# Kernel tuning notes

Hardware: AMD Instinct MI355X
Metric: run time of the kernel (lower is better)

The kernel has to match this reference:

```python
import jax, jax.numpy as jnp
import numpy as np

B, N, K, H, C = 16, 2048, 9, 128, 2  # K = nb_neighbors, kernel_size = K+1


def setup_inputs() -> dict:
    key = jax.random.key(0)
    ks = jax.random.split(key, 7)
    s = 0.1
    x = jax.random.normal(ks[0], (B, N, C), jnp.float32)
    Wconv = jax.random.normal(ks[1], (H, C, K + 1), jnp.float32) * s  # conv1d weight
    bconv = jax.random.normal(ks[2], (H,), jnp.float32) * s
    W1 = jax.random.normal(ks[3], (H, C), jnp.float32) * s
    b1 = jax.random.normal(ks[4], (H,), jnp.float32) * s
    W2 = jax.random.normal(ks[5], (H, H), jnp.float32) * s
    b2 = jax.random.normal(ks[6], (H,), jnp.float32) * s
    return {"x": x, "Wconv": Wconv, "bconv": bconv, "W1": W1, "b1": b1, "W2": W2, "b2": b2}


def reference(x, Wconv, bconv, W1, b1, W2, b2):
    # node embedding: W1(x)
    node_emb = jnp.einsum('bnc,hc->bnh', x, W1) + b1  # (B,N,H)

    # pairwise Euclidean distances (B,N,N) via the GEMM form
    sq = jnp.sum(x * x, axis=-1)  # (B,N)
    d2 = sq[:, :, None] + sq[:, None, :] - 2.0 * jnp.einsum('bnc,bmc->bnm', x, x)
    dist = jnp.sqrt(jnp.maximum(d2, 0.0))

    # torch: topk(k=N) (descending) then take last K+1 columns -> the K+1
    # smallest distances ordered descending (nearest/self last)
    knn = jnp.flip(jnp.argsort(dist, axis=-1)[..., : K + 1], axis=-1)  # (B,N,K+1)

    # batched gather of neighbor coords: (B,N,K+1,C)
    coords = jax.vmap(lambda xb, ib: xb[ib])(x, knn)

    # conv1d with kernel spanning the full window -> single output position,
    # i.e. a contraction over (channel, position)
    conv_emb = jnp.einsum('bnkc,hck->bnh', coords, Wconv) + bconv  # (B,N,H)
    conv_emb = jnp.einsum('bnh,eh->bne', conv_emb, W2) + b2

    return node_emb + conv_emb
```

## Files before the change

### kernel.cpp

```cpp
#include <hip/hip_runtime.h>
#include <cfloat>
#include <stdint.h>

#define B_   16
#define N_   2048
#define KK   10
#define H_   128
#define SUB  32
#define NCH  (N_ / SUB)

#define RANK_BLOCKS (B_ * 32)
#define WEFF_OUT    (H_ * KK * 2 + H_)
#define WEFF_BLOCKS ((WEFF_OUT * 4) / 256)

__device__ inline uint32_t f32_ordered(float f) {
    uint32_t u = __float_as_uint(f);
    return (u & 0x80000000u) ? ~u : (u | 0x80000000u);
}

__global__ __launch_bounds__(256) void setup_kernel(
    const float* __restrict__ x,
    const float* __restrict__ Wconv, const float* __restrict__ bconv,
    const float* __restrict__ b1,    const float* __restrict__ W2,
    const float* __restrict__ b2,
    float4* __restrict__ xsorted,
    float*  __restrict__ weff,
    float*  __restrict__ btot)
{
#pragma clang fp contract(off)
    __shared__ __align__(16) uint64_t sk[N_];
    __shared__ int pcnt[4 * 64];
    const int tid = threadIdx.x;

    if (blockIdx.x >= RANK_BLOCKS) {
        const int g = (blockIdx.x - RANK_BLOCKS) * 256 + tid;
        const int o = g >> 2, q = g & 3;
        float acc = 0.f;
        if (o < H_ * KK * 2) {
            const int e = o / 20, r = o % 20, k = r >> 1, c = r & 1;
            const float* w2p = W2 + e * H_ + q * 32;
            const float* wcp = Wconv + (q * 32) * (2 * KK) + c * KK + k;
#pragma unroll 8
            for (int h = 0; h < 32; ++h)
                acc += w2p[h] * wcp[h * (2 * KK)];
        } else {
            const int e = o - H_ * KK * 2;
            const float* w2p = W2 + e * H_ + q * 32;
            const float* bcp = bconv + q * 32;
#pragma unroll 8
            for (int h = 0; h < 32; ++h) acc += w2p[h] * bcp[h];
        }
        acc += __shfl_xor(acc, 1, 64);
        acc += __shfl_xor(acc, 2, 64);
        if (q == 0) {
            if (o < H_ * KK * 2) weff[o] = acc;
            else {
                const int e = o - H_ * KK * 2;
                btot[e] = acc + b1[e] + b2[e];
            }
        }
        return;
    }

    const int b  = blockIdx.x >> 5;
    const int sg = blockIdx.x & 31;
    const float2* xb = (const float2*)(x + (size_t)b * N_ * 2);

    for (int i = tid; i < N_; i += 256)
        sk[i] = ((uint64_t)f32_ordered(xb[i].x) << 32) | (uint32_t)i;
    __syncthreads();

    const int el = tid & 63;
    const int pt = tid >> 6;
    const uint64_t kown = sk[sg * 64 + el];
    const ulonglong2* sk2 = (const ulonglong2*)sk + pt * 256;
    int cnt = 0;
#pragma unroll 2
    for (int j = 0; j < 256; j += 4) {
        ulonglong2 t0 = sk2[j + 0];
        ulonglong2 t1 = sk2[j + 1];
        ulonglong2 t2 = sk2[j + 2];
        ulonglong2 t3 = sk2[j + 3];
        cnt += (int)(t0.x < kown) + (int)(t0.y < kown)
             + (int)(t1.x < kown) + (int)(t1.y < kown)
             + (int)(t2.x < kown) + (int)(t2.y < kown)
             + (int)(t3.x < kown) + (int)(t3.y < kown);
    }
    pcnt[pt * 64 + el] = cnt;
    __syncthreads();

    if (tid < 64) {
        const int r = pcnt[tid] + pcnt[64 + tid] + pcnt[128 + tid] + pcnt[192 + tid];
        const int i = sg * 64 + tid;
        float2 p = xb[i];
        float sm = p.x * p.x + p.y * p.y;
        xsorted[(size_t)b * N_ + r] =
            make_float4(p.x, p.y, sm, __uint_as_float((uint32_t)i));
    }
}

__global__ __launch_bounds__(512, 4) void knn_conv_kernel(
    const float4* __restrict__ xsorted,
    const float* __restrict__ W1,
    const float* __restrict__ weff,
    const float* __restrict__ btot,
    float* __restrict__ out)
{
#pragma clang fp contract(off)
    __shared__ float4 xs4[N_];
    __shared__ float  wcoord[64 * 21];

    const int tid  = threadIdx.x;
    const int w    = tid >> 6;
    const int r    = tid & 7;
    const int qm   = tid >> 3;
    const int b    = blockIdx.x >> 5;
    const int tile = blockIdx.x & 31;

    const float4* xb = xsorted + (size_t)b * N_;
    for (int i = tid; i < N_; i += 512) xs4[i] = xb[i];
    __syncthreads();

    const float4 qv = xs4[tile * 64 + qm];
    const float  qx = qv.x, qy = qv.y, sqn = qv.z;
    const int    gfirst = tile * 64 + w * 8;
    const float  qa  = xs4[gfirst].x;
    const float  qbx = xs4[gfirst + 7].x;

    const uint64_t KINIT = (((uint64_t)0x7F7FFFFFu) << 32) | 0x3FFFFFu;
    uint64_t hk[KK];
#pragma unroll
    for (int j = 0; j < KK; ++j) hk[j] = KINIT;
    float h9d  = FLT_MAX;
    float shb  = FLT_MAX;
    float gate = FLT_MAX;

    auto insert = [&](float dc, float cw, int m) {
        uint32_t oi = __float_as_uint(cw);
        uint64_t key = ((uint64_t)__float_as_uint(dc) << 32)
                     | (oi << 11) | (uint32_t)m;
        if (key < hk[KK - 1]) {
#pragma unroll
            for (int j = KK - 1; j >= 1; --j) {
                bool cj  = key < hk[j];
                bool cjm = key < hk[j - 1];
                hk[j] = cj ? (cjm ? hk[j - 1] : key) : hk[j];
            }
            hk[0] = (key < hk[0]) ? key : hk[0];
        }
        h9d  = __uint_as_float((uint32_t)(hk[KK - 1] >> 32));
        gate = fminf(h9d, shb);
    };

    auto scan_chunk = [&](int mc) {
        const int m0 = mc + r;
        float4 c0 = xs4[m0 + 0];
        float4 c1 = xs4[m0 + 8];
        float4 c2 = xs4[m0 + 16];
        float4 c3 = xs4[m0 + 24];
        float dc0, dc1, dc2, dc3;
        { float s = sqn + c0.z; float pr = qx * c0.x;
          float dt = __builtin_fmaf(qy, c0.y, pr);
          float d2 = __builtin_fmaf(-2.0f, dt, s); dc0 = d2 > 0.0f ? d2 : 0.0f; }
        { float s = sqn + c1.z; float pr = qx * c1.x;
          float dt = __builtin_fmaf(qy, c1.y, pr);
          float d2 = __builtin_fmaf(-2.0f, dt, s); dc1 = d2 > 0.0f ? d2 : 0.0f; }
        { float s = sqn + c2.z; float pr = qx * c2.x;
          float dt = __builtin_fmaf(qy, c2.y, pr);
          float d2 = __builtin_fmaf(-2.0f, dt, s); dc2 = d2 > 0.0f ? d2 : 0.0f; }
        { float s = sqn + c3.z; float pr = qx * c3.x;
          float dt = __builtin_fmaf(qy, c3.y, pr);
          float d2 = __builtin_fmaf(-2.0f, dt, s); dc3 = d2 > 0.0f ? d2 : 0.0f; }
        if (dc0 <= gate) insert(dc0, c0.w, m0 + 0);
        if (dc1 <= gate) insert(dc1, c1.w, m0 + 8);
        if (dc2 <= gate) insert(dc2, c2.w, m0 + 16);
        if (dc3 <= gate) insert(dc3, c3.w, m0 + 24);
    };

    auto bounds = [&]() {
        float gb = h9d;
        gb = fminf(gb, __shfl_xor(gb, 1, 64));
        gb = fminf(gb, __shfl_xor(gb, 2, 64));
        gb = fminf(gb, __shfl_xor(gb, 4, 64));
        float h1 = __uint_as_float((uint32_t)(hk[1] >> 32));
        h1 = fmaxf(h1, __shfl_xor(h1, 1, 64));
        h1 = fmaxf(h1, __shfl_xor(h1, 2, 64));
        h1 = fmaxf(h1, __shfl_xor(h1, 4, 64));
        shb  = fminf(shb, fminf(gb, h1));
        gate = fminf(h9d, shb);
        float wm = shb;
        wm = fmaxf(wm, __shfl_xor(wm, 8,  64));
        wm = fmaxf(wm, __shfl_xor(wm, 16, 64));
        wm = fmaxf(wm, __shfl_xor(wm, 32, 64));
        return wm;
    };

    const int home = tile * 2 + (w >> 2);
    int c0s = home - 1;
    if (c0s < 0) c0s = 0;
    if (c0s > NCH - 3) c0s = NCH - 3;
    scan_chunk((c0s + 0) * SUB);
    scan_chunk((c0s + 1) * SUB);
    scan_chunk((c0s + 2) * SUB);

    {
        uint64_t tc[KK];
#pragma unroll
        for (int j = 0; j < KK; ++j) tc[j] = hk[j];
        uint64_t last = 0;
#pragma unroll
        for (int sel = 0; sel < KK; ++sel) {
            uint64_t v  = tc[0];
            uint64_t t1 = __shfl_xor((unsigned long long)v, 1, 64);
            uint64_t m1 = v  < t1 ? v  : t1;
            uint64_t t2 = __shfl_xor((unsigned long long)m1, 2, 64);
            uint64_t m2 = m1 < t2 ? m1 : t2;
            uint64_t t4 = __shfl_xor((unsigned long long)m2, 4, 64);
            uint64_t vm = m2 < t4 ? m2 : t4;
            if (v == vm) {
#pragma unroll
                for (int j = 0; j < KK - 1; ++j) tc[j] = tc[j + 1];
                tc[KK - 1] = 0xFFFFFFFFFFFFFFFFull;
            }
            last = vm;
        }
        shb  = __uint_as_float((uint32_t)(last >> 32));
        gate = fminf(h9d, shb);
    }

    int  cl = c0s - 1, cr = c0s + 3;
    bool la = (cl >= 0), ra = (cr <= NCH - 1);
    while (la || ra) {
        float wm = bounds();
        if (la) {
            float gl = qa - xs4[cl * SUB + SUB - 1].x;
            if (__builtin_fmaf(gl, gl, -4e-6f) > wm) la = false;
            else { scan_chunk(cl * SUB); cl -= 1; la = (cl >= 0); }
        }
        if (ra) {
            float gr = xs4[cr * SUB].x - qbx;
            if (__builtin_fmaf(gr, gr, -4e-6f) > wm) ra = false;
            else { scan_chunk(cr * SUB); cr += 1; ra = (cr <= NCH - 1); }
        }
    }

    const int e = tid & 127;
    float we[20];
    {
        const float4* wp = (const float4*)(weff + e * 20);
#pragma unroll
        for (int rr = 0; rr < 5; ++rr) {
            float4 v = wp[rr];
            we[4 * rr + 0] = v.x; we[4 * rr + 1] = v.y;
            we[4 * rr + 2] = v.z; we[4 * rr + 3] = v.w;
        }
    }
    const float w1x = W1[e * 2 + 0];
    const float w1y = W1[e * 2 + 1];
    const float bt  = btot[e];

    {
#pragma unroll
        for (int sel = 0; sel < KK; ++sel) {
            uint64_t v  = hk[0];
            uint64_t t1 = __shfl_xor((unsigned long long)v, 1, 64);
            uint64_t m1 = v  < t1 ? v  : t1;
            uint64_t t2 = __shfl_xor((unsigned long long)m1, 2, 64);
            uint64_t m2 = m1 < t2 ? m1 : t2;
            uint64_t t4 = __shfl_xor((unsigned long long)m2, 4, 64);
            uint64_t vm = m2 < t4 ? m2 : t4;
            if (v == vm) {
#pragma unroll
                for (int j = 0; j < KK - 1; ++j) hk[j] = hk[j + 1];
                hk[KK - 1] = 0xFFFFFFFFFFFFFFFFull;
            }
            if (r == 0) {
                float4 c = xs4[(int)(vm & 0x7FF)];
                const int k = (KK - 1) - sel;
                wcoord[qm * 21 + 2 * k + 0] = c.x;
                wcoord[qm * 21 + 2 * k + 1] = c.y;
            }
        }
    }
    __syncthreads();

    const int qb_ = tid >> 7;
    const size_t obase = (size_t)b * N_ * H_;
#pragma unroll
    for (int jj = 0; jj < 16; ++jj) {
        const int qq = qb_ + 4 * jj;
        float4 xq = xs4[tile * 64 + qq];
        uint32_t orig = __float_as_uint(xq.w);
        const float* wc = &wcoord[qq * 21];
        float acc = bt;
        acc += xq.x * w1x;
        acc += xq.y * w1y;
#pragma unroll
        for (int k = 0; k < KK; ++k) {
            acc += wc[2 * k + 0] * we[2 * k + 0];
            acc += wc[2 * k + 1] * we[2 * k + 1];
        }
        out[obase + (size_t)orig * H_ + e] = acc;
    }
}

extern "C" void kernel_launch(void* const* d_in, const int* in_sizes, int n_in,
                              void* d_out, int out_size, void* d_ws, size_t ws_size,
                              hipStream_t stream) {
    const float* x     = (const float*)d_in[0];
    const float* Wconv = (const float*)d_in[1];
    const float* bconv = (const float*)d_in[2];
    const float* W1    = (const float*)d_in[3];
    const float* b1    = (const float*)d_in[4];
    const float* W2    = (const float*)d_in[5];
    const float* b2    = (const float*)d_in[6];
    float* out  = (float*)d_out;
    float* weff = (float*)d_ws;
    float* btot = weff + H_ * KK * 2;
    float4* xsorted = (float4*)((char*)d_ws + 16384);

    setup_kernel<<<dim3(RANK_BLOCKS + WEFF_BLOCKS), dim3(256), 0, stream>>>(
        x, Wconv, bconv, b1, W2, b2, xsorted, weff, btot);
    knn_conv_kernel<<<dim3(B_ * (N_ / 64)), dim3(512), 0, stream>>>(
        xsorted, W1, weff, btot, out);
}
```

Before: 143.6 us.

## Split each query's KNN scan across 16 lanes and halve queries per block

Each block now handles 32 queries instead of 64, with 16 lanes per query instead of 8, so the grid doubles and every lane scans half as many candidates per chunk. The wave reductions gain one extra shuffle stage to merge 16 partial top-K lists, and the launch bound asks for 8 waves per SIMD instead of 4. Sentinel keys now carry the lane id so they stay distinct during the merge. The goal is more parallelism and shorter per-lane serial insert chains, paid for by extra shuffle merges, more blocks each reloading the whole batch's points into shared memory, and tighter register limits.

After: 148.5 us. +3.4%, slower.

```diff
diff --git a/kernel.cpp b/kernel.cpp
--- a/kernel.cpp
+++ b/kernel.cpp
@@ -99,7 +99,7 @@
     }
 }
 
-__global__ __launch_bounds__(512, 4) void knn_conv_kernel(
+__global__ __launch_bounds__(512, 8) void knn_conv_kernel(
     const float4* __restrict__ xsorted,
     const float* __restrict__ W1,
     const float* __restrict__ weff,
@@ -108,29 +108,30 @@
 {
 #pragma clang fp contract(off)
     __shared__ float4 xs4[N_];
-    __shared__ float  wcoord[64 * 21];
+    __shared__ float  wcoord[32 * 21];
 
     const int tid  = threadIdx.x;
     const int w    = tid >> 6;
-    const int r    = tid & 7;
-    const int qm   = tid >> 3;
-    const int b    = blockIdx.x >> 5;
-    const int tile = blockIdx.x & 31;
+    const int l    = tid & 63;
+    const int r    = tid & 15;
+    const int qm   = tid >> 4;
+    const int b    = blockIdx.x >> 6;
+    const int tile = blockIdx.x & 63;
 
     const float4* xb = xsorted + (size_t)b * N_;
     for (int i = tid; i < N_; i += 512) xs4[i] = xb[i];
     __syncthreads();
 
-    const float4 qv = xs4[tile * 64 + qm];
+    const float4 qv = xs4[tile * 32 + qm];
     const float  qx = qv.x, qy = qv.y, sqn = qv.z;
-    const int    gfirst = tile * 64 + w * 8;
+    const int    gfirst = tile * 32 + w * 4;
     const float  qa  = xs4[gfirst].x;
-    const float  qbx = xs4[gfirst + 7].x;
-
-    const uint64_t KINIT = (((uint64_t)0x7F7FFFFFu) << 32) | 0x3FFFFFu;
+    const float  qbx = xs4[gfirst + 3].x;
+
+    const uint64_t KSENT = (((uint64_t)0x7F7FFFFFu) << 32) | 0x400000u | (uint32_t)l;
     uint64_t hk[KK];
 #pragma unroll
-    for (int j = 0; j < KK; ++j) hk[j] = KINIT;
+    for (int j = 0; j < KK; ++j) hk[j] = KSENT;
     float h9d  = FLT_MAX;
     float shb  = FLT_MAX;
     float gate = FLT_MAX;
@@ -155,26 +156,16 @@
     auto scan_chunk = [&](int mc) {
         const int m0 = mc + r;
         float4 c0 = xs4[m0 + 0];
-        float4 c1 = xs4[m0 + 8];
-        float4 c2 = xs4[m0 + 16];
-        float4 c3 = xs4[m0 + 24];
-        float dc0, dc1, dc2, dc3;
+        float4 c1 = xs4[m0 + 16];
+        float dc0, dc1;
         { float s = sqn + c0.z; float pr = qx * c0.x;
           float dt = __builtin_fmaf(qy, c0.y, pr);
           float d2 = __builtin_fmaf(-2.0f, dt, s); dc0 = d2 > 0.0f ? d2 : 0.0f; }
         { float s = sqn + c1.z; float pr = qx * c1.x;
           float dt = __builtin_fmaf(qy, c1.y, pr);
           float d2 = __builtin_fmaf(-2.0f, dt, s); dc1 = d2 > 0.0f ? d2 : 0.0f; }
-        { float s = sqn + c2.z; float pr = qx * c2.x;
-          float dt = __builtin_fmaf(qy, c2.y, pr);
-          float d2 = __builtin_fmaf(-2.0f, dt, s); dc2 = d2 > 0.0f ? d2 : 0.0f; }
-        { float s = sqn + c3.z; float pr = qx * c3.x;
-          float dt = __builtin_fmaf(qy, c3.y, pr);
-          float d2 = __builtin_fmaf(-2.0f, dt, s); dc3 = d2 > 0.0f ? d2 : 0.0f; }
         if (dc0 <= gate) insert(dc0, c0.w, m0 + 0);
-        if (dc1 <= gate) insert(dc1, c1.w, m0 + 8);
-        if (dc2 <= gate) insert(dc2, c2.w, m0 + 16);
-        if (dc3 <= gate) insert(dc3, c3.w, m0 + 24);
+        if (dc1 <= gate) insert(dc1, c1.w, m0 + 16);
     };
 
     auto bounds = [&]() {
@@ -182,21 +173,21 @@
         gb = fminf(gb, __shfl_xor(gb, 1, 64));
         gb = fminf(gb, __shfl_xor(gb, 2, 64));
         gb = fminf(gb, __shfl_xor(gb, 4, 64));
+        gb = fminf(gb, __shfl_xor(gb, 8, 64));
         float h1 = __uint_as_float((uint32_t)(hk[1] >> 32));
         h1 = fmaxf(h1, __shfl_xor(h1, 1, 64));
         h1 = fmaxf(h1, __shfl_xor(h1, 2, 64));
         h1 = fmaxf(h1, __shfl_xor(h1, 4, 64));
+        h1 = fmaxf(h1, __shfl_xor(h1, 8, 64));
         shb  = fminf(shb, fminf(gb, h1));
         gate = fminf(h9d, shb);
         float wm = shb;
-        wm = fmaxf(wm, __shfl_xor(wm, 8,  64));
         wm = fmaxf(wm, __shfl_xor(wm, 16, 64));
         wm = fmaxf(wm, __shfl_xor(wm, 32, 64));
         return wm;
     };
 
-    const int home = tile * 2 + (w >> 2);
-    int c0s = home - 1;
+    int c0s = tile - 1;
     if (c0s < 0) c0s = 0;
     if (c0s > NCH - 3) c0s = NCH - 3;
     scan_chunk((c0s + 0) * SUB);
@@ -216,7 +207,9 @@
             uint64_t t2 = __shfl_xor((unsigned long long)m1, 2, 64);
             uint64_t m2 = m1 < t2 ? m1 : t2;
             uint64_t t4 = __shfl_xor((unsigned long long)m2, 4, 64);
-            uint64_t vm = m2 < t4 ? m2 : t4;
+            uint64_t m4 = m2 < t4 ? m2 : t4;
+            uint64_t t8 = __shfl_xor((unsigned long long)m4, 8, 64);
+            uint64_t vm = m4 < t8 ? m4 : t8;
             if (v == vm) {
 #pragma unroll
                 for (int j = 0; j < KK - 1; ++j) tc[j] = tc[j + 1];
@@ -268,7 +261,9 @@
             uint64_t t2 = __shfl_xor((unsigned long long)m1, 2, 64);
             uint64_t m2 = m1 < t2 ? m1 : t2;
             uint64_t t4 = __shfl_xor((unsigned long long)m2, 4, 64);
-            uint64_t vm = m2 < t4 ? m2 : t4;
+            uint64_t m4 = m2 < t4 ? m2 : t4;
+            uint64_t t8 = __shfl_xor((unsigned long long)m4, 8, 64);
+            uint64_t vm = m4 < t8 ? m4 : t8;
             if (v == vm) {
 #pragma unroll
                 for (int j = 0; j < KK - 1; ++j) hk[j] = hk[j + 1];
@@ -287,9 +282,9 @@
     const int qb_ = tid >> 7;
     const size_t obase = (size_t)b * N_ * H_;
 #pragma unroll
-    for (int jj = 0; jj < 16; ++jj) {
+    for (int jj = 0; jj < 8; ++jj) {
         const int qq = qb_ + 4 * jj;
-        float4 xq = xs4[tile * 64 + qq];
+        float4 xq = xs4[tile * 32 + qq];
         uint32_t orig = __float_as_uint(xq.w);
         const float* wc = &wcoord[qq * 21];
         float acc = bt;
@@ -321,6 +316,6 @@
 
     setup_kernel<<<dim3(RANK_BLOCKS + WEFF_BLOCKS), dim3(256), 0, stream>>>(
         x, Wconv, bconv, b1, W2, b2, xsorted, weff, btot);
-    knn_conv_kernel<<<dim3(B_ * (N_ / 64)), dim3(512), 0, stream>>>(
+    knn_conv_kernel<<<dim3(B_ * NCH), dim3(512), 0, stream>>>(
         xsorted, W1, weff, btot, out);
 }
```

## Seed KNN heap by sorting initial 12 candidates; skip final selection if unchanged

Applied to the files above, without the earlier changes.

Each lane now seeds its top-K heap by computing the first three chunks' 12 candidate keys at once and sorting them in registers with an odd-even transposition network, replacing 12 sequential guarded insertions. The first cross-lane merge now also writes the neighbor coordinates. The second merge-and-write pass runs only if some lane inserted during the expansion phase, tracked with a flag and a wave ballot. This removes serial insert chains and a redundant merge in the common case, at the cost of extra register pressure from the 12-element array.

Measured after the change: 143.3 us. About the same (-0.2%).

```diff
diff --git a/kernel.cpp b/kernel.cpp
--- a/kernel.cpp
+++ b/kernel.cpp
@@ -127,13 +127,11 @@
     const float  qa  = xs4[gfirst].x;
     const float  qbx = xs4[gfirst + 7].x;
 
-    const uint64_t KINIT = (((uint64_t)0x7F7FFFFFu) << 32) | 0x3FFFFFu;
     uint64_t hk[KK];
-#pragma unroll
-    for (int j = 0; j < KK; ++j) hk[j] = KINIT;
     float h9d  = FLT_MAX;
     float shb  = FLT_MAX;
     float gate = FLT_MAX;
+    bool  p2ins = false;
 
     auto insert = [&](float dc, float cw, int m) {
         uint32_t oi = __float_as_uint(cw);
@@ -147,6 +145,7 @@
                 hk[j] = cj ? (cjm ? hk[j - 1] : key) : hk[j];
             }
             hk[0] = (key < hk[0]) ? key : hk[0];
+            p2ins = true;
         }
         h9d  = __uint_as_float((uint32_t)(hk[KK - 1] >> 32));
         gate = fminf(h9d, shb);
@@ -199,9 +198,63 @@
     int c0s = home - 1;
     if (c0s < 0) c0s = 0;
     if (c0s > NCH - 3) c0s = NCH - 3;
-    scan_chunk((c0s + 0) * SUB);
-    scan_chunk((c0s + 1) * SUB);
-    scan_chunk((c0s + 2) * SUB);
+    {
+        const int m0 = c0s * SUB + r;
+        uint64_t k12[12];
+#pragma unroll
+        for (int ch = 0; ch < 3; ++ch) {
+            const int mb = m0 + ch * SUB;
+            float4 c0 = xs4[mb + 0];
+            float4 c1 = xs4[mb + 8];
+            float4 c2 = xs4[mb + 16];
+            float4 c3 = xs4[mb + 24];
+            float dc0, dc1, dc2, dc3;
+            { float s = sqn + c0.z; float pr = qx * c0.x;
+              float dt = __builtin_fmaf(qy, c0.y, pr);
+              float d2 = __builtin_fmaf(-2.0f, dt, s); dc0 = d2 > 0.0f ? d2 : 0.0f; }
+            { float s = sqn + c1.z; float pr = qx * c1.x;
+              float dt = __builtin_fmaf(qy, c1.y, pr);
+              float d2 = __builtin_fmaf(-2.0f, dt, s); dc1 = d2 > 0.0f ? d2 : 0.0f; }
+            { float s = sqn + c2.z; float pr = qx * c2.x;
+              float dt = __builtin_fmaf(qy, c2.y, pr);
+              float d2 = __builtin_fmaf(-2.0f, dt, s); dc2 = d2 > 0.0f ? d2 : 0.0f; }
+            { float s = sqn + c3.z; float pr = qx * c3.x;
+              float dt = __builtin_fmaf(qy, c3.y, pr);
+              float d2 = __builtin_fmaf(-2.0f, dt, s); dc3 = d2 > 0.0f ? d2 : 0.0f; }
+            k12[ch * 4 + 0] = ((uint64_t)__float_as_uint(dc0) << 32)
+                            | (__float_as_uint(c0.w) << 11) | (uint32_t)(mb + 0);
+            k12[ch * 4 + 1] = ((uint64_t)__float_as_uint(dc1) << 32)
+                            | (__float_as_uint(c1.w) << 11) | (uint32_t)(mb + 8);
+            k12[ch * 4 + 2] = ((uint64_t)__float_as_uint(dc2) << 32)
+                            | (__float_as_uint(c2.w) << 11) | (uint32_t)(mb + 16);
+            k12[ch * 4 + 3] = ((uint64_t)__float_as_uint(dc3) << 32)
+                            | (__float_as_uint(c3.w) << 11) | (uint32_t)(mb + 24);
+        }
+#pragma unroll
+        for (int rnd = 0; rnd < 12; ++rnd) {
+            if ((rnd & 1) == 0) {
+#pragma unroll
+                for (int i = 0; i < 12; i += 2) {
+                    uint64_t a = k12[i], bk = k12[i + 1];
+                    bool lt = a < bk;
+                    k12[i]     = lt ? a  : bk;
+                    k12[i + 1] = lt ? bk : a;
+                }
+            } else {
+#pragma unroll
+                for (int i = 1; i < 11; i += 2) {
+                    uint64_t a = k12[i], bk = k12[i + 1];
+                    bool lt = a < bk;
+                    k12[i]     = lt ? a  : bk;
+                    k12[i + 1] = lt ? bk : a;
+                }
+            }
+        }
+#pragma unroll
+        for (int j = 0; j < KK; ++j) hk[j] = k12[j];
+        h9d  = __uint_as_float((uint32_t)(hk[KK - 1] >> 32));
+        gate = h9d;
+    }
 
     {
         uint64_t tc[KK];
@@ -222,6 +275,12 @@
                 for (int j = 0; j < KK - 1; ++j) tc[j] = tc[j + 1];
                 tc[KK - 1] = 0xFFFFFFFFFFFFFFFFull;
             }
+            if (r == 0) {
+                float4 c = xs4[(int)(vm & 0x7FF)];
+                const int k = (KK - 1) - sel;
+                wcoord[qm * 21 + 2 * k + 0] = c.x;
+                wcoord[qm * 21 + 2 * k + 1] = c.y;
+            }
             last = vm;
         }
         shb  = __uint_as_float((uint32_t)(last >> 32));
@@ -259,7 +318,7 @@
     const float w1y = W1[e * 2 + 1];
     const float bt  = btot[e];
 
-    {
+    if (__ballot(p2ins)) {
 #pragma unroll
         for (int sel = 0; sel < KK; ++sel) {
             uint64_t v  = hk[0];
```
